# Kernel tuning notes

Hardware: AMD Instinct MI355X
Metric: run time of the kernel (lower is better)

Reference implementation:

```python
import jax, jax.numpy as jnp
import numpy as np

L, M, N = 28, 28, 28   # lateral slices, rows, cols (fixed by the tNN module)
BATCH = 65536


def setup_inputs() -> dict:
    key = jax.random.key(0)
    k1, k2, k3 = jax.random.split(key, 3)
    x = jax.random.normal(k1, (L, N, BATCH), dtype=jnp.float32)
    W = jax.random.normal(k2, (L, M, N), dtype=jnp.float32)
    B = jax.random.normal(k3, (L, M, 1), dtype=jnp.float32)
    return {"x": x, "W": W, "B": B}


def t_product(A, X):
    """t-product: out[k] = sum_j A[(k-j) mod l] @ X[j].
    Equivalent to fold(bcirc(A) @ unfold(X)) as in torch_tensor_product,
    but exploits the circulant structure instead of materializing the
    (l*m, l*n) block-circulant matrix."""
    l = A.shape[0]
    idx = (jnp.arange(l)[:, None] - jnp.arange(l)[None, :]) % l  # [k, j]
    Ar = A[idx]  # (l, l, m, n) -- small: l^2 * m * n elements
    return jnp.einsum('kjmn,jnp->kmp', Ar, X)  # (l, m, p)


def reference(x, W, B):
    # forward: relu(W * x + B) with * the tensor t-product
    return jax.nn.relu(t_product(W, x) + B)
```

## Files before the change

kernel.cpp:

```cpp
#include <hip/hip_runtime.h>


typedef __attribute__((ext_vector_type(4))) float f32x4;
typedef __attribute__((ext_vector_type(8))) short s16x8;
typedef __attribute__((ext_vector_type(4))) unsigned int u32x4;

#define BATCH    65536
#define MROWS    784
#define KDIM     784
#define KSTEPS   25
#define BM       112
#define BN       256
#define MT       7
#define NT       256
#define NWG      (MT*NT)
#define ATILE_ELEMS 3584
#define AWS_ELEMS  (MT*KSTEPS*ATILE_ELEMS)

__device__ __forceinline__ unsigned int rne1(float f) {
  unsigned int u = __float_as_uint(f);
  return (u + 0x7fffu + ((u >> 16) & 1u)) >> 16;
}
__device__ __forceinline__ unsigned int pack2(float a, float b) {
  return rne1(a) | (rne1(b) << 16);
}

typedef const __attribute__((address_space(1))) unsigned int glb_uint;
typedef __attribute__((address_space(3))) unsigned int lds_uint;
__device__ __forceinline__ void async16(const void* g, void* l) {
  __builtin_amdgcn_global_load_lds((glb_uint*)g, (lds_uint*)l, 16, 0, 0);
}

__global__ void build_A(const float* __restrict__ W, unsigned short* __restrict__ A_ws) {
  int idx = blockIdx.x * 256 + threadIdx.x;
  if (idx >= AWS_ELEMS) return;
  int tile = idx / ATILE_ELEMS;
  int o    = idx - tile * ATILE_ELEMS;
  int mt   = tile / KSTEPS;
  int ks   = tile - mt * KSTEPS;
  int e    = o & 7;
  int slot = o >> 3;
  int kb   = slot / BM;
  int ml   = slot - kb * BM;
  int r    = mt * BM + ml;
  int c    = ks * 32 + kb * 8 + e;
  float v = 0.0f;
  if (c < KDIM) {
    int kl = r / 28, mm = r - kl * 28;
    int j  = c / 28, n  = c - j * 28;
    int d = kl - j; if (d < 0) d += 28;
    v = W[(d * 28 + mm) * 28 + n];
  }
  A_ws[idx] = (unsigned short)rne1(v);
}

__global__ __launch_bounds__(256, 2) void tnn_gemm(
    const float* __restrict__ X, const unsigned short* __restrict__ A_ws,
    const float* __restrict__ Bias, float* __restrict__ C) {
  __shared__ __align__(16) unsigned short a_lds[ATILE_ELEMS];
  __shared__ __align__(16) unsigned short x_lds[8192];

  int bid = blockIdx.x;
  int wg  = (bid & 7) * (NWG / 8) + (bid >> 3);
  int nt  = wg / MT;
  int mt  = wg - nt * MT;

  int tid  = threadIdx.x;
  int lane = tid & 63;
  int wave = tid >> 6;

  f32x4 acc[7][4];
#pragma unroll
  for (int i = 0; i < 7; ++i)
#pragma unroll
    for (int j = 0; j < 4; ++j)
      acc[i][j] = (f32x4){0.f, 0.f, 0.f, 0.f};

  const float* xbase = X + (size_t)(nt * BN) + ((size_t)(wave * 8) << 16) + (lane << 2);
  int wslot0 = wave * 256 + (lane << 2);

  int a_rd    = (((lane >> 4) * BM) + (lane & 15)) * 16;
  int x_slot0 = (lane >> 4) * 256 + wave * 64 + (lane & 15);

  for (int ks = 0; ks < KSTEPS; ++ks) {
    f32x4 v[8];
    int k0 = ks * 32 + wave * 8;
    const float* xs = xbase + ((size_t)ks << 21);
#pragma unroll
    for (int dk = 0; dk < 8; ++dk) {
      if (k0 + dk < KDIM) v[dk] = *(const f32x4*)(xs + ((size_t)dk << 16));
      else                v[dk] = (f32x4){0.f, 0.f, 0.f, 0.f};
    }

    __syncthreads();

    const unsigned short* atile = A_ws + (size_t)(mt * KSTEPS + ks) * ATILE_ELEMS;
    async16(atile + wave * 512 + lane * 8, &a_lds[wave * 512]);
    if (wave < 3)
      async16(atile + (wave + 4) * 512 + lane * 8, &a_lds[(wave + 4) * 512]);

#pragma unroll
    for (int di = 0; di < 4; ++di) {
      int slot = wslot0 + di;
      int boff = (slot * 16) ^ (((slot >> 5) & 7) << 4);
      u32x4 w;
      w.x = pack2(v[0][di], v[1][di]);
      w.y = pack2(v[2][di], v[3][di]);
      w.z = pack2(v[4][di], v[5][di]);
      w.w = pack2(v[6][di], v[7][di]);
      *(u32x4*)((char*)x_lds + boff) = w;
    }

    __syncthreads();

    s16x8 af[7], xf[4];
#pragma unroll
    for (int i = 0; i < 7; ++i)
      af[i] = *(const s16x8*)((const char*)a_lds + a_rd + i * 256);
#pragma unroll
    for (int jn = 0; jn < 4; ++jn) {
      int slot = x_slot0 + jn * 16;
      int boff = (slot * 16) ^ (((slot >> 5) & 7) << 4);
      xf[jn] = *(const s16x8*)((const char*)x_lds + boff);
    }
#pragma unroll
    for (int i = 0; i < 7; ++i)
#pragma unroll
      for (int jn = 0; jn < 4; ++jn)
        acc[i][jn] = __builtin_amdgcn_mfma_f32_16x16x32_bf16(af[i], xf[jn], acc[i][jn], 0, 0, 0);
  }

  int colbase = nt * BN + wave * 64 + (lane & 15);
#pragma unroll
  for (int i = 0; i < 7; ++i) {
    int r0 = mt * BM + i * 16 + ((lane >> 4) << 2);
    f32x4 bv = *(const f32x4*)&Bias[r0];
#pragma unroll
    for (int jn = 0; jn < 4; ++jn) {
      size_t cb = ((size_t)r0 << 16) + (size_t)(colbase + jn * 16);
#pragma unroll
      for (int d = 0; d < 4; ++d) {
        float vv = acc[i][jn][d] + bv[d];
        C[cb + ((size_t)d << 16)] = fmaxf(vv, 0.0f);
      }
    }
  }
}

extern "C" void kernel_launch(void* const* d_in, const int* in_sizes, int n_in,
                              void* d_out, int out_size, void* d_ws, size_t ws_size,
                              hipStream_t stream) {
  const float* x  = (const float*)d_in[0];
  const float* W  = (const float*)d_in[1];
  const float* B  = (const float*)d_in[2];
  float* out = (float*)d_out;
  unsigned short* A_ws = (unsigned short*)d_ws;

  build_A<<<(AWS_ELEMS + 255) / 256, 256, 0, stream>>>(W, A_ws);
  tnn_gemm<<<NWG, 256, 0, stream>>>(x, A_ws, B, out);
}
```

Measured before the change: 466.9 us.

## Pre-convert X to tiled bf16 workspace and load both operands via async LDS copies

Adds a pre-pass kernel that converts the fp32 input X into bf16 tiles already laid out for the GEMM's LDS format. The new GEMM then loads both A and X tiles straight into LDS with async global-to-LDS copies, with no per-workgroup fp32 loads and conversion. The old kernel re-read and re-converted each X tile in all 7 M-tile workgroups. The cost is an extra kernel launch plus a ~100 MB bf16 workspace write and read, and the new path runs only if the workspace is large enough.

```diff
diff --git a/kernel.cpp b/kernel.cpp
--- a/kernel.cpp
+++ b/kernel.cpp
@@ -16,6 +16,9 @@
 #define NWG      (MT*NT)
 #define ATILE_ELEMS 3584
 #define AWS_ELEMS  (MT*KSTEPS*ATILE_ELEMS)
+#define XTILE_ELEMS 8192
+#define XWS_ELEMS  ((size_t)NT*KSTEPS*XTILE_ELEMS)
+#define WS_NEED    ((AWS_ELEMS + XWS_ELEMS) * 2)
 
 __device__ __forceinline__ unsigned int rne1(float f) {
   unsigned int u = __float_as_uint(f);
@@ -54,6 +57,105 @@
   A_ws[idx] = (unsigned short)rne1(v);
 }
 
+__global__ void convert_x(const float* __restrict__ X, unsigned short* __restrict__ Xw) {
+  int gid = blockIdx.x * 256 + threadIdx.x;
+  int tile   = gid >> 10;
+  int within = gid & 1023;
+  int kb = within >> 8, n = within & 255;
+  int nt = tile / KSTEPS, ks = tile - nt * KSTEPS;
+  int k0 = ks * 32 + kb * 8;
+  const float* src = X + (size_t)k0 * BATCH + nt * BN + n;
+  float v[8];
+  if (k0 + 7 < KDIM) {
+#pragma unroll
+    for (int e = 0; e < 8; ++e) v[e] = src[(size_t)e << 16];
+  } else {
+#pragma unroll
+    for (int e = 0; e < 8; ++e) v[e] = (k0 + e < KDIM) ? src[(size_t)e << 16] : 0.0f;
+  }
+  u32x4 w;
+  w.x = pack2(v[0], v[1]);
+  w.y = pack2(v[2], v[3]);
+  w.z = pack2(v[4], v[5]);
+  w.w = pack2(v[6], v[7]);
+  *(u32x4*)(Xw + ((size_t)gid << 3)) = w;
+}
+
+__global__ __launch_bounds__(256, 2) void tnn_gemm2(
+    const unsigned short* __restrict__ A_ws, const unsigned short* __restrict__ X_ws,
+    const float* __restrict__ Bias, float* __restrict__ C) {
+  __shared__ __align__(16) unsigned short a_lds[ATILE_ELEMS];
+  __shared__ __align__(16) unsigned short x_lds[XTILE_ELEMS];
+
+  int bid = blockIdx.x;
+  int wg  = (bid & 7) * (NWG / 8) + (bid >> 3);
+  int nt  = wg / MT;
+  int mt  = wg - nt * MT;
+
+  int tid  = threadIdx.x;
+  int lane = tid & 63;
+  int wave = tid >> 6;
+
+  f32x4 acc[7][4];
+#pragma unroll
+  for (int i = 0; i < 7; ++i)
+#pragma unroll
+    for (int j = 0; j < 4; ++j)
+      acc[i][j] = (f32x4){0.f, 0.f, 0.f, 0.f};
+
+  int a_rd    = (((lane >> 4) * BM) + (lane & 15)) * 16;
+  int x_rd    = ((lane >> 4) * 256 + wave * 64 + (lane & 15)) * 16;
+
+  const unsigned short* abase = A_ws + (size_t)mt * KSTEPS * ATILE_ELEMS;
+  const unsigned short* xbase = X_ws + (size_t)nt * KSTEPS * XTILE_ELEMS;
+
+  for (int ks = 0; ks < KSTEPS; ++ks) {
+    __syncthreads();
+
+    const unsigned short* at = abase + ks * ATILE_ELEMS;
+    async16(at + wave * 512 + lane * 8, &a_lds[wave * 512]);
+    if (wave < 3)
+      async16(at + (wave + 4) * 512 + lane * 8, &a_lds[(wave + 4) * 512]);
+
+    const unsigned short* xt = xbase + ks * XTILE_ELEMS;
+#pragma unroll
+    for (int c = 0; c < 4; ++c)
+      async16(xt + wave * 2048 + c * 512 + lane * 8,
+              &x_lds[wave * 2048 + c * 512]);
+
+    __syncthreads();
+
+    s16x8 af[7], xf[4];
+#pragma unroll
+    for (int i = 0; i < 7; ++i)
+      af[i] = *(const s16x8*)((const char*)a_lds + a_rd + i * 256);
+#pragma unroll
+    for (int jn = 0; jn < 4; ++jn)
+      xf[jn] = *(const s16x8*)((const char*)x_lds + x_rd + jn * 256);
+#pragma unroll
+    for (int i = 0; i < 7; ++i)
+#pragma unroll
+      for (int jn = 0; jn < 4; ++jn)
+        acc[i][jn] = __builtin_amdgcn_mfma_f32_16x16x32_bf16(af[i], xf[jn], acc[i][jn], 0, 0, 0);
+  }
+
+  int colbase = nt * BN + wave * 64 + (lane & 15);
+#pragma unroll
+  for (int i = 0; i < 7; ++i) {
+    int r0 = mt * BM + i * 16 + ((lane >> 4) << 2);
+    f32x4 bv = *(const f32x4*)&Bias[r0];
+#pragma unroll
+    for (int jn = 0; jn < 4; ++jn) {
+      size_t cb = ((size_t)r0 << 16) + (size_t)(colbase + jn * 16);
+#pragma unroll
+      for (int d = 0; d < 4; ++d) {
+        float vv = acc[i][jn][d] + bv[d];
+        C[cb + ((size_t)d << 16)] = fmaxf(vv, 0.0f);
+      }
+    }
+  }
+}
+
 __global__ __launch_bounds__(256, 2) void tnn_gemm(
     const float* __restrict__ X, const unsigned short* __restrict__ A_ws,
     const float* __restrict__ Bias, float* __restrict__ C) {
@@ -64,7 +166,6 @@
   int wg  = (bid & 7) * (NWG / 8) + (bid >> 3);
   int nt  = wg / MT;
   int mt  = wg - nt * MT;
-
   int tid  = threadIdx.x;
   int lane = tid & 63;
   int wave = tid >> 6;
@@ -78,7 +179,6 @@
 
   const float* xbase = X + (size_t)(nt * BN) + ((size_t)(wave * 8) << 16) + (lane << 2);
   int wslot0 = wave * 256 + (lane << 2);
-
   int a_rd    = (((lane >> 4) * BM) + (lane & 15)) * 16;
   int x_slot0 = (lane >> 4) * 256 + wave * 64 + (lane & 15);
 
@@ -91,14 +191,11 @@
       if (k0 + dk < KDIM) v[dk] = *(const f32x4*)(xs + ((size_t)dk << 16));
       else                v[dk] = (f32x4){0.f, 0.f, 0.f, 0.f};
     }
-
-    __syncthreads();
-
+    __syncthreads();
     const unsigned short* atile = A_ws + (size_t)(mt * KSTEPS + ks) * ATILE_ELEMS;
     async16(atile + wave * 512 + lane * 8, &a_lds[wave * 512]);
     if (wave < 3)
       async16(atile + (wave + 4) * 512 + lane * 8, &a_lds[(wave + 4) * 512]);
-
 #pragma unroll
     for (int di = 0; di < 4; ++di) {
       int slot = wslot0 + di;
@@ -110,9 +207,7 @@
       w.w = pack2(v[6][di], v[7][di]);
       *(u32x4*)((char*)x_lds + boff) = w;
     }
-
-    __syncthreads();
-
+    __syncthreads();
     s16x8 af[7], xf[4];
 #pragma unroll
     for (int i = 0; i < 7; ++i)
@@ -155,7 +250,13 @@
   const float* B  = (const float*)d_in[2];
   float* out = (float*)d_out;
   unsigned short* A_ws = (unsigned short*)d_ws;
+  unsigned short* X_ws = A_ws + AWS_ELEMS;
 
   build_A<<<(AWS_ELEMS + 255) / 256, 256, 0, stream>>>(W, A_ws);
-  tnn_gemm<<<NWG, 256, 0, stream>>>(x, A_ws, B, out);
-}
+  if (ws_size >= WS_NEED) {
+    convert_x<<<(int)(XWS_ELEMS / 8 / 256), 256, 0, stream>>>(x, X_ws);
+    tnn_gemm2<<<NWG, 256, 0, stream>>>(A_ws, X_ws, B, out);
+  } else {
+    tnn_gemm<<<NWG, 256, 0, stream>>>(x, A_ws, B, out);
+  }
+}
```

After: 467.1 us. Within noise of the previous version (+0.0%).
